# Optimization experiments

Measured on AMD Instinct MI355X. Metric: run time of the kernel, lower is better.

The kernel has to match this reference:

```python
import jax, jax.numpy as jnp
import numpy as np

N_NODES = 1024
HID = 128
NODE_D = 133
BOND_D = 14
E_HALF = 8192  # directed edges; doubled with reverses -> 16384


def setup_inputs() -> dict:
    key = jax.random.key(0)
    ks = jax.random.split(key, 24)

    x = jax.random.normal(ks[0], (N_NODES, NODE_D), jnp.float32)
    edge_attr = jax.random.normal(ks[1], (2 * E_HALF, BOND_D), jnp.float32)
    src = jax.random.randint(ks[2], (E_HALF,), 0, N_NODES)
    dst = jax.random.randint(ks[3], (E_HALF,), 0, N_NODES)
    # bidirectional edges so every edge has a reverse (as _rev_edge_index assumes)
    edge_index = jnp.stack([jnp.concatenate([src, dst]), jnp.concatenate([dst, src])]).astype(jnp.int32)
    rev_edge_index = jnp.concatenate([jnp.arange(E_HALF) + E_HALF, jnp.arange(E_HALF)]).astype(jnp.int32)

    dissociable_masks = (jax.random.uniform(ks[4], (N_NODES,)) < 0.1).astype(jnp.int32)
    pka_raw = jax.random.uniform(ks[5], (N_NODES,), minval=0.0, maxval=14.0)
    valid = jax.random.uniform(ks[6], (N_NODES,)) < (1.0 / 16.0)
    pka_values = jnp.where(valid, pka_raw, jnp.nan).astype(jnp.float32)

    def lin(k, fi, fo):
        return (jax.random.normal(k, (fi, fo)) / np.sqrt(fi)).astype(jnp.float32)

    z = lambda n: jnp.zeros((n,), jnp.float32)
    inp = dict(x=x, edge_attr=edge_attr, pka_values=pka_values,
               dissociable_masks=dissociable_masks, edge_index=edge_index,
               rev_edge_index=rev_edge_index,
               Wi=lin(ks[7], NODE_D + BOND_D, HID), bi=z(HID),
               Wh=lin(ks[8], HID, HID), bh=z(HID),
               Wo=lin(ks[9], NODE_D + HID, HID), bo=z(HID),
               Wnt=lin(ks[10], NODE_D, HID), bnt=z(HID),
               Wc1=lin(ks[11], HID, 256), bc1=z(256),
               Wc2=lin(ks[12], 256, 64), bc2=z(64),
               Wc3=lin(ks[13], 64, 2), bc3=z(2),
               Wr1=lin(ks[14], HID, 256), br1=z(256),
               Wr2=lin(ks[15], 256, 64), br2=z(64),
               Wr3=lin(ks[16], 64, 1), br3=z(1),
               Wg=lin(ks[17], HID, HID), bg=z(HID))
    return inp


def reference(x, edge_attr, pka_values, dissociable_masks, edge_index, rev_edge_index,
              Wi, bi, Wh, bh, Wo, bo, Wnt, bnt,
              Wc1, bc1, Wc2, bc2, Wc3, bc3,
              Wr1, br1, Wr2, br2, Wr3, br3, Wg, bg):
    n = x.shape[0]
    src, dst = edge_index[0], edge_index[1]

    # ---- BondMessagePassing (depth=3, dropout in eval mode) ----
    H0 = jnp.concatenate([x[src], edge_attr], axis=1) @ Wi + bi  # [E, HID]
    Ht = jax.nn.relu(H0)
    for _ in range(2):  # depth - 1 iterations
        agg = jax.ops.segment_sum(Ht, dst, num_segments=n)       # scatter-sum to dst
        M = agg[src] - Ht[rev_edge_index]                        # exclude reverse edge
        Ht = jax.nn.relu(H0 + M @ Wh + bh)
    agg = jax.ops.segment_sum(Ht, dst, num_segments=n)
    tx = x @ Wnt + bnt
    M = jnp.where(jnp.sum(agg, axis=1, keepdims=True) == 0, tx, agg)
    E = jax.nn.relu(jnp.concatenate([x, M], axis=1) @ Wo + bo)   # node embeddings [N, HID]

    valid = ~jnp.isnan(pka_values)
    pka_s = jnp.where(valid, pka_values, 0.0)

    def mlp(e, W1, b1, W2, b2, W3, b3):
        h = jax.nn.relu(e @ W1 + b1)
        h = jax.nn.relu(h @ W2 + b2)
        return h @ W3 + b3

    def step(carry, inp):
        Emb, cls_sum, reg_sum, correct = carry
        i, m_i, p_i, v_i = inp
        e = Emb[i]
        logits = mlp(e, Wc1, bc1, Wc2, bc2, Wc3, bc3)            # [2]
        label = jnp.argmax(logits).astype(jnp.int32)
        target = (m_i > 0).astype(jnp.int32)
        ce = -jax.nn.log_softmax(logits)[target]
        correct = correct + (label == target).astype(jnp.float32)
        reg_cond = (label == 1) | (m_i > 0)
        # sigmoid -> Hardtanh(0,14) (clip is identity on (0,1), kept for fidelity)
        p = jnp.clip(jax.nn.sigmoid(mlp(e, Wr1, br1, Wr2, br2, Wr3, br3))[0], 0.0, 14.0)
        fire = reg_cond & v_i
        reg_sum = reg_sum + jnp.where(fire, (p - p_i) ** 2, 0.0)
        Emb = jax.lax.cond(fire,
                           lambda A: A * (1.0 - jax.nn.sigmoid(A @ Wg + bg)),
                           lambda A: A, Emb)
        return (Emb, cls_sum + ce, reg_sum, correct), (label, jnp.where(reg_cond, p, 0.0))

    init = (E, jnp.float32(0.0), jnp.float32(0.0), jnp.float32(0.0))
    xs = (jnp.arange(n), dissociable_masks, pka_s, valid)
    (_, cls_sum, reg_sum, correct), (labels, preds) = jax.lax.scan(step, init, xs)
    acc = jax.lax.stop_gradient(correct / n)
    loss_vec = jnp.stack([cls_sum + reg_sum, cls_sum, reg_sum, acc])
    return labels, preds, loss_vec
```

## Files before the change

kernel.cpp:

```cpp
#include <hip/hip_runtime.h>

#define NN   1024
#define NE   16384
#define HID  128
#define ND   133
#define BD   14
#define KIN  147
#define NVMAX 128
#define EB   8
#define JF   4
#define JT   2
#define MAXPAIRS (NVMAX * (NVMAX + 1) / 2)
#define TB4 ((MAXPAIRS + JT - 1) / JT)

__device__ __forceinline__ float sigm(float x) { return 1.0f / (1.0f + expf(-x)); }


__global__ void __launch_bounds__(1024)
k_prep3(const int* __restrict__ dst, int* offs, int* elist,
        const float* __restrict__ pka, int* validIdx, int* NvP, int* vpos,
        const int* __restrict__ mask, int* pairCnt, int* pairList,
        int* lossTicket) {
    __shared__ int degS[NN];
    __shared__ int s2[NN];
    __shared__ int fillS[NN];
    __shared__ int elistS[NE];
    __shared__ int vIdxS[NVMAX];
    __shared__ int maskS[NVMAX];
    __shared__ int nvS, pcS;
    int t = threadIdx.x;
    degS[t] = 0;
    float v = pka[t];
    int f = (v == v) ? 1 : 0;
    s2[t] = f;
    __syncthreads();
    for (int e = t; e < NE; e += NN) atomicAdd(&degS[dst[e]], 1);
    __syncthreads();
    int d0 = degS[t];
    __syncthreads();
    for (int st = 1; st < NN; st <<= 1) {
        int a = (t >= st) ? degS[t - st] : 0;
        int b = (t >= st) ? s2[t - st] : 0;
        __syncthreads();
        degS[t] += a; s2[t] += b;
        __syncthreads();
    }
    int hi = degS[t];
    int lo = hi - d0;
    offs[t] = lo;
    fillS[t] = lo;
    if (t == NN - 1) offs[NN] = hi;
    int pos = s2[t] - f;
    int ok = (f && pos < NVMAX) ? 1 : 0;
    vpos[t] = ok ? pos : -1;
    if (ok) { validIdx[pos] = t; vIdxS[pos] = t; }
    if (t == NN - 1) { int nv = (s2[t] > NVMAX) ? NVMAX : s2[t]; *NvP = nv; nvS = nv; }
    if (t == 0) { pcS = 0; *lossTicket = 0; }
    __syncthreads();
    for (int e = t; e < NE; e += NN) { int p = atomicAdd(&fillS[dst[e]], 1); elistS[p] = e; }
    int Nv = nvS;
    if (t < NVMAX) maskS[t] = (t < Nv) ? mask[vIdxS[t]] : 1;
    __syncthreads();
    for (int a = lo + 1; a < hi; a++) {
        int vv = elistS[a]; int b = a - 1;
        while (b >= lo && elistS[b] > vv) { elistS[b + 1] = elistS[b]; b--; }
        elistS[b + 1] = vv;
    }
    for (int idx = t; idx < NVMAX * NVMAX; idx += NN) {
        int vv = idx >> 7, k = idx & (NVMAX - 1);
        if (vv < Nv && k <= vv && maskS[vv] == 0) {
            int p = atomicAdd(&pcS, 1);
            pairList[p] = idx;
        }
    }
    __syncthreads();
    if (t == 0) *pairCnt = pcS;
    for (int e = t; e < NE; e += NN) elist[e] = elistS[e];
}


__global__ void k_edge_init(const float* __restrict__ x, const float* __restrict__ ea,
                            const int* __restrict__ src,
                            const float* __restrict__ Wi, const float* __restrict__ bi,
                            float* __restrict__ H0, float* __restrict__ Ht) {
    __shared__ float in[EB][KIN + 1];
    int e0 = blockIdx.x * EB;
    int h = threadIdx.x;
    for (int j = 0; j < EB; j++) {
        int e = e0 + j; int s = src[e];
        for (int k = h; k < KIN; k += HID)
            in[j][k] = (k < ND) ? x[s * ND + k] : ea[e * BD + (k - ND)];
    }
    __syncthreads();
    float acc[EB];
#pragma unroll
    for (int j = 0; j < EB; j++) acc[j] = 0.f;
    for (int k4 = 0; k4 < KIN / 4; k4++) {
        float w0 = Wi[(4 * k4 + 0) * HID + h];
        float w1 = Wi[(4 * k4 + 1) * HID + h];
        float w2 = Wi[(4 * k4 + 2) * HID + h];
        float w3 = Wi[(4 * k4 + 3) * HID + h];
#pragma unroll
        for (int j = 0; j < EB; j++) {
            const float4 m4 = *(const float4*)&in[j][4 * k4];
            acc[j] = fmaf(m4.x, w0, acc[j]);
            acc[j] = fmaf(m4.y, w1, acc[j]);
            acc[j] = fmaf(m4.z, w2, acc[j]);
            acc[j] = fmaf(m4.w, w3, acc[j]);
        }
    }
    for (int k = (KIN / 4) * 4; k < KIN; k++) {
        float w = Wi[k * HID + h];
#pragma unroll
        for (int j = 0; j < EB; j++) acc[j] = fmaf(in[j][k], w, acc[j]);
    }
    float b = bi[h];
    for (int j = 0; j < EB; j++) {
        float v = acc[j] + b;
        H0[(e0 + j) * HID + h] = v;
        Ht[(e0 + j) * HID + h] = fmaxf(v, 0.f);
    }
}

__global__ void k_segsum(const float* __restrict__ Ht, const int* __restrict__ elist,
                         const int* __restrict__ offs, float* __restrict__ agg) {
    int n = blockIdx.x; int h = threadIdx.x;
    int lo = offs[n], hi = offs[n + 1];
    float a = 0.f;
    for (int j = lo; j < hi; j++) {
        int e = elist[j];
        a += Ht[e * HID + h];
    }
    agg[n * HID + h] = a;
}

__global__ void k_edge_update(const float* __restrict__ H0, const float* __restrict__ Htin,
                              const float* __restrict__ agg,
                              const int* __restrict__ src, const int* __restrict__ rev,
                              const float* __restrict__ Wh, const float* __restrict__ bh,
                              float* __restrict__ Htout) {
    __shared__ float M[EB][HID];
    int e0 = blockIdx.x * EB;
    int h = threadIdx.x;
    for (int j = 0; j < EB; j++) {
        int e = e0 + j; int s = src[e]; int r = rev[e];
        M[j][h] = agg[s * HID + h] - Htin[r * HID + h];
    }
    __syncthreads();
    float acc[EB];
#pragma unroll
    for (int j = 0; j < EB; j++) acc[j] = 0.f;
    for (int k4 = 0; k4 < HID / 4; k4++) {
        float w0 = Wh[(4 * k4 + 0) * HID + h];
        float w1 = Wh[(4 * k4 + 1) * HID + h];
        float w2 = Wh[(4 * k4 + 2) * HID + h];
        float w3 = Wh[(4 * k4 + 3) * HID + h];
#pragma unroll
        for (int j = 0; j < EB; j++) {
            const float4 m4 = *(const float4*)&M[j][4 * k4];
            acc[j] = fmaf(m4.x, w0, acc[j]);
            acc[j] = fmaf(m4.y, w1, acc[j]);
            acc[j] = fmaf(m4.z, w2, acc[j]);
            acc[j] = fmaf(m4.w, w3, acc[j]);
        }
    }
    float b = bh[h];
    for (int j = 0; j < EB; j++) {
        int e = e0 + j;
        Htout[e * HID + h] = fmaxf(H0[e * HID + h] + acc[j] + b, 0.f);
    }
}

__global__ void k_node_embed2(const float* __restrict__ x, const float* __restrict__ Ht,
                              const int* __restrict__ elist, const int* __restrict__ offs,
                              const float* __restrict__ Wnt, const float* __restrict__ bnt,
                              const float* __restrict__ Wo, const float* __restrict__ bo,
                              float* __restrict__ Emb) {
    __shared__ float xs[ND + 1];
    __shared__ float Ms[HID];
    __shared__ float red[HID];
    int n = blockIdx.x; int h = threadIdx.x;
    for (int k = h; k < ND; k += HID) xs[k] = x[n * ND + k];
    int lo = offs[n], hi = offs[n + 1];
    float a = 0.f;
    for (int j = lo; j < hi; j++) a += Ht[elist[j] * HID + h];
    red[h] = a;
    __syncthreads();
    for (int st = 64; st > 0; st >>= 1) { if (h < st) red[h] += red[h + st]; __syncthreads(); }
    float s = red[0];
    __syncthreads();
    float Mh;
    if (s == 0.0f) {
        float t0 = 0.f, t1 = 0.f;
        int k = 0;
        for (; k + 1 < ND; k += 2) {
            t0 = fmaf(xs[k], Wnt[k * HID + h], t0);
            t1 = fmaf(xs[k + 1], Wnt[(k + 1) * HID + h], t1);
        }
        for (; k < ND; k++) t0 = fmaf(xs[k], Wnt[k * HID + h], t0);
        Mh = (t0 + t1) + bnt[h];
    } else {
        Mh = a;
    }
    Ms[h] = Mh;
    __syncthreads();
    float a0 = 0.f, a1 = 0.f;
    int k = 0;
    for (; k + 1 < ND; k += 2) {
        a0 = fmaf(xs[k], Wo[k * HID + h], a0);
        a1 = fmaf(xs[k + 1], Wo[(k + 1) * HID + h], a1);
    }
    for (; k < ND; k++) a0 = fmaf(xs[k], Wo[k * HID + h], a0);
    for (int q = 0; q < HID; q += 2) {
        a0 = fmaf(Ms[q], Wo[(ND + q) * HID + h], a0);
        a1 = fmaf(Ms[q + 1], Wo[(ND + q + 1) * HID + h], a1);
    }
    Emb[n * HID + h] = fmaxf((a0 + a1) + bo[h], 0.f);
}


__global__ void __launch_bounds__(512)
k_chains3(const float* __restrict__ Emb, const int* __restrict__ validIdx,
          const int* __restrict__ NvP,
          const float* __restrict__ Wg, const float* __restrict__ bg,
          float* __restrict__ specSt) {
    int v = blockIdx.x;
    int Nv = *NvP;
    if (v >= Nv) return;
    __shared__ float rS[HID];
    __shared__ float pS[512];
    int tid = threadIdx.x;
    int col = tid & (HID - 1);
    int slot = tid >> 7;
    float wreg[32];
#pragma unroll
    for (int q = 0; q < 32; q++)
        wreg[q] = Wg[(slot * 32 + q) * HID + col];
    float bgc = bg[col];
    int i = validIdx[v];
    if (tid < HID) rS[tid] = Emb[i * HID + tid];
    __syncthreads();
    if (slot == 0) specSt[(size_t)(v * NVMAX + 0) * HID + col] = rS[col];
    int kmax = (v < NVMAX - 1) ? v : (NVMAX - 1);
    for (int k = 1; k <= kmax; k++) {
        const float4* r4 = (const float4*)&rS[slot * 32];
        float px = 0.f, py = 0.f, pz = 0.f, pw = 0.f;
#pragma unroll
        for (int q8 = 0; q8 < 8; q8++) {
            float4 rr = r4[q8];
            px = fmaf(rr.x, wreg[4 * q8 + 0], px);
            py = fmaf(rr.y, wreg[4 * q8 + 1], py);
            pz = fmaf(rr.z, wreg[4 * q8 + 2], pz);
            pw = fmaf(rr.w, wreg[4 * q8 + 3], pw);
        }
        pS[tid] = (px + py) + (pz + pw);
        __syncthreads();
        if (slot == 0) {
            float s = ((pS[col] + pS[col + 128]) + (pS[col + 256] + pS[col + 384])) + bgc;
            float g = 1.0f - sigm(s);
            float nr = rS[col] * g;
            rS[col] = nr;
            specSt[(size_t)(v * NVMAX + k) * HID + col] = nr;
        }
        __syncthreads();
    }
}


__global__ void __launch_bounds__(256)
k_table4(const float* __restrict__ specSt, const int* __restrict__ pairList,
         const int* __restrict__ pairCnt,
         const float* __restrict__ Wc1, const float* __restrict__ bc1,
         const float* __restrict__ Wc2, const float* __restrict__ bc2,
         const float* __restrict__ Wc3, const float* __restrict__ bc3,
         int* __restrict__ labTab) {
    int cnt = *pairCnt;
    int base = blockIdx.x * JT;
    if (base >= cnt) return;
    int nj = cnt - base; if (nj > JT) nj = JT;
    __shared__ float rS[JT][HID];
    __shared__ float h1S[JT][256];
    __shared__ float h2S[JT][64];
    __shared__ int plS[JT];
    int tid = threadIdx.x;
    if (tid < JT) plS[tid] = (tid < nj) ? pairList[base + tid] : 0;
    __syncthreads();
    for (int idx = tid; idx < JT * HID; idx += 256) {
        int j = idx >> 7, k = idx & (HID - 1);
        rS[j][k] = (j < nj) ? specSt[(size_t)plS[j] * HID + k] : 0.f;
    }
    __syncthreads();
    {
        float a[JT];
#pragma unroll
        for (int j = 0; j < JT; j++) a[j] = 0.f;
        for (int k = 0; k < HID; k++) {
            float w = Wc1[k * 256 + tid];
#pragma unroll
            for (int j = 0; j < JT; j++) a[j] = fmaf(rS[j][k], w, a[j]);
        }
        float b1 = bc1[tid];
#pragma unroll
        for (int j = 0; j < JT; j++) h1S[j][tid] = fmaxf(a[j] + b1, 0.f);
    }
    __syncthreads();
    {
        int col = tid & 63, j = tid >> 6;
        if (j < nj) {
            float acc = 0.f;
            for (int k = 0; k < 256; k++)
                acc = fmaf(h1S[j][k], Wc2[k * 64 + col], acc);
            h2S[j][col] = fmaxf(acc + bc2[col], 0.f);
        }
    }
    __syncthreads();
    if (tid < nj) {
        float l0 = bc3[0], l1 = bc3[1];
        for (int k = 0; k < 64; k++) {
            float h = h2S[tid][k];
            l0 = fmaf(h, Wc3[2 * k + 0], l0);
            l1 = fmaf(h, Wc3[2 * k + 1], l1);
        }
        labTab[plS[tid]] = (l1 > l0) ? 1 : 0;
    }
}


__global__ void k_resolve2(const int* __restrict__ validIdx, const int* __restrict__ NvP,
                           const int* __restrict__ mask, const int* __restrict__ labTab,
                           int* fireFlag, int* kPref) {
    __shared__ int vIdxS[NVMAX];
    __shared__ int maskS[NVMAX];
    __shared__ int labS[NVMAX * NVMAX];
    __shared__ int fireS[NN];
    __shared__ int scanS[NN];
    int t = threadIdx.x;
    int Nv = *NvP;
    if (t < NVMAX) {
        int vi = (t < Nv) ? validIdx[t] : 0;
        vIdxS[t] = vi;
        maskS[t] = (t < Nv) ? mask[vi] : 0;
    }
    fireS[t] = 0;
    for (int idx = t; idx < Nv * NVMAX; idx += NN) labS[idx] = labTab[idx];
    __syncthreads();
    if (t == 0) {
        int k = 0;
        for (int v = 0; v < Nv; v++) {
            int fire = (maskS[v] > 0) ? 1 : labS[v * NVMAX + k];
            fireS[vIdxS[v]] = fire;
            k += fire;
        }
    }
    __syncthreads();
    int f0 = fireS[t];
    scanS[t] = f0;
    __syncthreads();
    for (int st = 1; st < NN; st <<= 1) {
        int u = (t >= st) ? scanS[t - st] : 0;
        __syncthreads();
        scanS[t] += u;
        __syncthreads();
    }
    kPref[t] = scanS[t] - f0;
    fireFlag[t] = f0;
}


__global__ void __launch_bounds__(256)
k_final8(const float* __restrict__ Emb, const int* __restrict__ kPref,
         const int* __restrict__ fireFlag, const int* __restrict__ mask,
         const float* __restrict__ pka, const int* __restrict__ vpos,
         const int* __restrict__ labTab,
         const float* __restrict__ Wg, const float* __restrict__ bg,
         const float* __restrict__ Wc1, const float* __restrict__ bc1,
         const float* __restrict__ Wc2, const float* __restrict__ bc2,
         const float* __restrict__ Wc3, const float* __restrict__ bc3,
         const float* __restrict__ Wr1, const float* __restrict__ br1,
         const float* __restrict__ Wr2, const float* __restrict__ br2,
         const float* __restrict__ Wr3, const float* __restrict__ br3,
         float* __restrict__ outLabels, float* __restrict__ outPreds,
         float* __restrict__ ceArr, float* __restrict__ regArr,
         float* __restrict__ corArr, float* __restrict__ outLoss,
         int* __restrict__ lossTicket) {
    __shared__ __align__(16) float WgS[HID * HID];
    __shared__ __align__(16) float rS[JF][HID];
    __shared__ __align__(16) float pS[JF][8][HID];
    __shared__ float h1S[JF][256];
    __shared__ float h2S[JF][64];
    __shared__ float lgS[JF][2];
    __shared__ float prS[JF];
    __shared__ int kcS[JF];
    __shared__ int tkS;
    int tid = threadIdx.x;
    int i0 = blockIdx.x * JF;

    const float4* Wg4 = (const float4*)Wg;
    float4* Ws4 = (float4*)WgS;
    for (int idx = tid; idx < HID * HID / 4; idx += 256) Ws4[idx] = Wg4[idx];
    if (tid < HID) {
#pragma unroll
        for (int j = 0; j < JF; j++) rS[j][tid] = Emb[(i0 + j) * HID + tid];
    }
    if (tid < JF) kcS[tid] = kPref[i0 + tid];
    __syncthreads();
    int kc[JF]; int maxkc = 0;
#pragma unroll
    for (int j = 0; j < JF; j++) { kc[j] = kcS[j]; if (kc[j] > maxkc) maxkc = kc[j]; }

    int cg = tid & 31;
    int qs = tid >> 5;
    int q0 = qs * 16;
    int rc = tid & (HID - 1);
    int rh = tid >> 7;
    float bgc = bg[rc];
    const float4* WgS4 = (const float4*)WgS;
    for (int t = 0; t < maxkc; t++) {
        float4 acc[JF];
#pragma unroll
        for (int j = 0; j < JF; j++) acc[j] = make_float4(0.f, 0.f, 0.f, 0.f);
        for (int qq = 0; qq < 16; qq += 4) {
            int q = q0 + qq;
            const float4 w0 = WgS4[(q + 0) * 32 + cg];
            const float4 w1 = WgS4[(q + 1) * 32 + cg];
            const float4 w2 = WgS4[(q + 2) * 32 + cg];
            const float4 w3 = WgS4[(q + 3) * 32 + cg];
#pragma unroll
            for (int j = 0; j < JF; j++) {
                const float4 r = *(const float4*)&rS[j][q];
                acc[j].x = fmaf(r.x, w0.x, acc[j].x);
                acc[j].x = fmaf(r.y, w1.x, acc[j].x);
                acc[j].x = fmaf(r.z, w2.x, acc[j].x);
                acc[j].x = fmaf(r.w, w3.x, acc[j].x);
                acc[j].y = fmaf(r.x, w0.y, acc[j].y);
                acc[j].y = fmaf(r.y, w1.y, acc[j].y);
                acc[j].y = fmaf(r.z, w2.y, acc[j].y);
                acc[j].y = fmaf(r.w, w3.y, acc[j].y);
                acc[j].z = fmaf(r.x, w0.z, acc[j].z);
                acc[j].z = fmaf(r.y, w1.z, acc[j].z);
                acc[j].z = fmaf(r.z, w2.z, acc[j].z);
                acc[j].z = fmaf(r.w, w3.z, acc[j].z);
                acc[j].w = fmaf(r.x, w0.w, acc[j].w);
                acc[j].w = fmaf(r.y, w1.w, acc[j].w);
                acc[j].w = fmaf(r.z, w2.w, acc[j].w);
                acc[j].w = fmaf(r.w, w3.w, acc[j].w);
            }
        }
#pragma unroll
        for (int j = 0; j < JF; j++)
            *(float4*)&pS[j][qs][4 * cg] = acc[j];
        __syncthreads();
        float nr0, nr1;
        {
            int j = 2 * rh;
            float s = pS[j][0][rc];
#pragma unroll
            for (int z = 1; z < 8; z++) s += pS[j][z][rc];
            float g = 1.0f - sigm(s + bgc);
            nr0 = (t < kc[j]) ? rS[j][rc] * g : rS[j][rc];
        }
        {
            int j = 2 * rh + 1;
            float s = pS[j][0][rc];
#pragma unroll
            for (int z = 1; z < 8; z++) s += pS[j][z][rc];
            float g = 1.0f - sigm(s + bgc);
            nr1 = (t < kc[j]) ? rS[j][rc] * g : rS[j][rc];
        }
        __syncthreads();
        rS[2 * rh][rc] = nr0;
        rS[2 * rh + 1][rc] = nr1;
        __syncthreads();
    }

    {
        float a[JF];
#pragma unroll
        for (int j = 0; j < JF; j++) a[j] = 0.f;
        for (int k = 0; k < HID; k++) {
            float w = Wc1[k * 256 + tid];
#pragma unroll
            for (int j = 0; j < JF; j++) a[j] = fmaf(rS[j][k], w, a[j]);
        }
        float b = bc1[tid];
#pragma unroll
        for (int j = 0; j < JF; j++) h1S[j][tid] = fmaxf(a[j] + b, 0.f);
    }
    __syncthreads();
    {
        int c2 = tid & 63, j = tid >> 6;
        float acc = 0.f;
        for (int k = 0; k < 256; k++) acc = fmaf(h1S[j][k], Wc2[k * 64 + c2], acc);
        h2S[j][c2] = fmaxf(acc + bc2[c2], 0.f);
    }
    __syncthreads();
    if (tid < 2 * JF) {
        int j = tid >> 1, c = tid & 1;
        float l = bc3[c];
        for (int k = 0; k < 64; k++) l = fmaf(h2S[j][k], Wc3[2 * k + c], l);
        lgS[j][c] = l;
    }
    __syncthreads();

    {
        float a[JF];
#pragma unroll
        for (int j = 0; j < JF; j++) a[j] = 0.f;
        for (int k = 0; k < HID; k++) {
            float w = Wr1[k * 256 + tid];
#pragma unroll
            for (int j = 0; j < JF; j++) a[j] = fmaf(rS[j][k], w, a[j]);
        }
        float b = br1[tid];
#pragma unroll
        for (int j = 0; j < JF; j++) h1S[j][tid] = fmaxf(a[j] + b, 0.f);
    }
    __syncthreads();
    {
        int c2 = tid & 63, j = tid >> 6;
        float acc = 0.f;
        for (int k = 0; k < 256; k++) acc = fmaf(h1S[j][k], Wr2[k * 64 + c2], acc);
        h2S[j][c2] = fmaxf(acc + br2[c2], 0.f);
    }
    __syncthreads();
    if (tid < JF) {
        float pr = br3[0];
        for (int k = 0; k < 64; k++) pr = fmaf(h2S[tid][k], Wr3[k], pr);
        prS[tid] = pr;
    }
    __syncthreads();

    if (tid < JF) {
        int j = tid, i = i0 + j;
        float l0 = lgS[j][0], l1 = lgS[j][1];
        int compLab = (l1 > l0) ? 1 : 0;
        int vp = vpos[i];
        int label = (vp >= 0 && mask[i] == 0) ? labTab[vp * NVMAX + kc[j]] : compLab;
        int target = (mask[i] > 0) ? 1 : 0;
        float mx = fmaxf(l0, l1);
        float lse = mx + logf(expf(l0 - mx) + expf(l1 - mx));
        float ce = lse - ((target == 1) ? l1 : l0);
        int reg_cond = (label == 1) || (mask[i] > 0);
        float p = sigm(prS[j]);
        p = fminf(fmaxf(p, 0.f), 14.f);
        outLabels[i] = (float)label;
        outPreds[i] = reg_cond ? p : 0.f;
        ceArr[i] = ce;
        corArr[i] = (label == target) ? 1.f : 0.f;
        if (fireFlag[i]) {
            float d = p - pka[i];
            regArr[i] = d * d;
        } else {
            regArr[i] = 0.f;
        }
    }

    __threadfence();
    __syncthreads();
    if (tid == 0) tkS = atomicAdd(lossTicket, 1);
    __syncthreads();
    if (tkS == (NN / JF) - 1) {
        __threadfence();
        __shared__ float s[256];
        float a = ((ceArr[tid] + ceArr[tid + 256]) + (ceArr[tid + 512] + ceArr[tid + 768]));
        s[tid] = a; __syncthreads();
        for (int st = 128; st > 0; st >>= 1) { if (tid < st) s[tid] += s[tid + st]; __syncthreads(); }
        float cls = s[0]; __syncthreads();
        a = ((regArr[tid] + regArr[tid + 256]) + (regArr[tid + 512] + regArr[tid + 768]));
        s[tid] = a; __syncthreads();
        for (int st = 128; st > 0; st >>= 1) { if (tid < st) s[tid] += s[tid + st]; __syncthreads(); }
        float reg = s[0]; __syncthreads();
        a = ((corArr[tid] + corArr[tid + 256]) + (corArr[tid + 512] + corArr[tid + 768]));
        s[tid] = a; __syncthreads();
        for (int st = 128; st > 0; st >>= 1) { if (tid < st) s[tid] += s[tid + st]; __syncthreads(); }
        float cor = s[0];
        if (tid == 0) {
            outLoss[0] = cls + reg;
            outLoss[1] = cls;
            outLoss[2] = reg;
            outLoss[3] = cor / (float)NN;
        }
    }
}


extern "C" void kernel_launch(void* const* d_in, const int* in_sizes, int n_in,
                              void* d_out, int out_size, void* d_ws, size_t ws_size,
                              hipStream_t stream) {
    const float* x    = (const float*)d_in[0];
    const float* ea   = (const float*)d_in[1];
    const float* pka  = (const float*)d_in[2];
    const int*   mask = (const int*)d_in[3];
    const int*   eidx = (const int*)d_in[4];
    const int*   rev  = (const int*)d_in[5];
    const float* Wi  = (const float*)d_in[6];  const float* bi  = (const float*)d_in[7];
    const float* Wh  = (const float*)d_in[8];  const float* bh  = (const float*)d_in[9];
    const float* Wo  = (const float*)d_in[10]; const float* bo  = (const float*)d_in[11];
    const float* Wnt = (const float*)d_in[12]; const float* bnt = (const float*)d_in[13];
    const float* Wc1 = (const float*)d_in[14]; const float* bc1 = (const float*)d_in[15];
    const float* Wc2 = (const float*)d_in[16]; const float* bc2 = (const float*)d_in[17];
    const float* Wc3 = (const float*)d_in[18]; const float* bc3 = (const float*)d_in[19];
    const float* Wr1 = (const float*)d_in[20]; const float* br1 = (const float*)d_in[21];
    const float* Wr2 = (const float*)d_in[22]; const float* br2 = (const float*)d_in[23];
    const float* Wr3 = (const float*)d_in[24]; const float* br3 = (const float*)d_in[25];
    const float* Wg  = (const float*)d_in[26]; const float* bg  = (const float*)d_in[27];

    const int* src = eidx;
    const int* dst = eidx + NE;

    char* w = (char*)d_ws;
    auto alloc = [&](size_t bytes) -> void* {
        void* p = (void*)w;
        w += ((bytes + 255) / 256) * 256;
        return p;
    };
    float* H0   = (float*)alloc((size_t)NE * HID * 4);
    float* HtA  = (float*)alloc((size_t)NE * HID * 4);
    float* HtB  = (float*)alloc((size_t)NE * HID * 4);
    float* agg  = (float*)alloc((size_t)NN * HID * 4);
    float* Emb  = (float*)alloc((size_t)NN * HID * 4);
    int* offs    = (int*)alloc((NN + 1) * 4);
    int* elist   = (int*)alloc(NE * 4);
    int* validIdx= (int*)alloc(NVMAX * 4);
    int* NvP     = (int*)alloc(16);
    int* vpos    = (int*)alloc(NN * 4);
    int* fireFlag= (int*)alloc(NN * 4);
    int* kPref   = (int*)alloc(NN * 4);
    float* specSt= (float*)alloc((size_t)NVMAX * NVMAX * HID * 4);
    int* labTab  = (int*)alloc(NVMAX * NVMAX * 4);
    int* pairCnt = (int*)alloc(16);
    int* pairList= (int*)alloc(MAXPAIRS * 4);
    int* lossTicket = (int*)alloc(16);
    float* ceArr = (float*)alloc(NN * 4);
    float* regArr= (float*)alloc(NN * 4);
    float* corArr= (float*)alloc(NN * 4);

    float* outF = (float*)d_out;

    k_prep3<<<1, NN, 0, stream>>>(dst, offs, elist, pka, validIdx, NvP, vpos,
                                  mask, pairCnt, pairList, lossTicket);

    k_edge_init<<<NE / EB, HID, 0, stream>>>(x, ea, src, Wi, bi, H0, HtA);
    k_segsum<<<NN, HID, 0, stream>>>(HtA, elist, offs, agg);
    k_edge_update<<<NE / EB, HID, 0, stream>>>(H0, HtA, agg, src, rev, Wh, bh, HtB);
    k_segsum<<<NN, HID, 0, stream>>>(HtB, elist, offs, agg);
    k_edge_update<<<NE / EB, HID, 0, stream>>>(H0, HtB, agg, src, rev, Wh, bh, HtA);
    k_node_embed2<<<NN, HID, 0, stream>>>(x, HtA, elist, offs, Wnt, bnt, Wo, bo, Emb);

    k_chains3<<<NVMAX, 512, 0, stream>>>(Emb, validIdx, NvP, Wg, bg, specSt);
    k_table4<<<TB4, 256, 0, stream>>>(specSt, pairList, pairCnt,
                                      Wc1, bc1, Wc2, bc2, Wc3, bc3, labTab);
    k_resolve2<<<1, NN, 0, stream>>>(validIdx, NvP, mask, labTab, fireFlag, kPref);

    k_final8<<<NN / JF, 256, 0, stream>>>(Emb, kPref, fireFlag, mask, pka, vpos, labTab,
                                          Wg, bg, Wc1, bc1, Wc2, bc2, Wc3, bc3,
                                          Wr1, br1, Wr2, br2, Wr3, br3,
                                          outF, outF + NN, ceArr, regArr, corArr,
                                          outF + 2 * NN, lossTicket);
}
```

Baseline: 215.5 us.

## Double block size in final kernel and double-buffer gating state to drop a barrier

The final per-node kernel now runs 512 threads per block instead of 256. Each half of the block computes the gated matvec for two of the four nodes, and the first MLP layer is split the same way. The gating state is double-buffered, so each serial gating step needs two barriers instead of three. The aim is to shorten the serial chain of gating steps by spreading it over more threads. The cost is larger shared-memory use per block and some idle threads in the layers that stay 256-wide.

Result: slower. 225.5 us (+4.7%).

```diff
diff --git a/kernel.cpp b/kernel.cpp
--- a/kernel.cpp
+++ b/kernel.cpp
@@ -367,8 +367,8 @@
 }
 
 
-__global__ void __launch_bounds__(256)
-k_final8(const float* __restrict__ Emb, const int* __restrict__ kPref,
+__global__ void __launch_bounds__(512)
+k_final9(const float* __restrict__ Emb, const int* __restrict__ kPref,
          const int* __restrict__ fireFlag, const int* __restrict__ mask,
          const float* __restrict__ pka, const int* __restrict__ vpos,
          const int* __restrict__ labTab,
@@ -384,7 +384,7 @@
          float* __restrict__ corArr, float* __restrict__ outLoss,
          int* __restrict__ lossTicket) {
     __shared__ __align__(16) float WgS[HID * HID];
-    __shared__ __align__(16) float rS[JF][HID];
+    __shared__ __align__(16) float rs[2][JF][HID];
     __shared__ __align__(16) float pS[JF][8][HID];
     __shared__ float h1S[JF][256];
     __shared__ float h2S[JF][64];
@@ -397,10 +397,10 @@
 
     const float4* Wg4 = (const float4*)Wg;
     float4* Ws4 = (float4*)WgS;
-    for (int idx = tid; idx < HID * HID / 4; idx += 256) Ws4[idx] = Wg4[idx];
+    for (int idx = tid; idx < HID * HID / 4; idx += 512) Ws4[idx] = Wg4[idx];
     if (tid < HID) {
 #pragma unroll
-        for (int j = 0; j < JF; j++) rS[j][tid] = Emb[(i0 + j) * HID + tid];
+        for (int j = 0; j < JF; j++) rs[0][j][tid] = Emb[(i0 + j) * HID + tid];
     }
     if (tid < JF) kcS[tid] = kPref[i0 + tid];
     __syncthreads();
@@ -408,86 +408,80 @@
 #pragma unroll
     for (int j = 0; j < JF; j++) { kc[j] = kcS[j]; if (kc[j] > maxkc) maxkc = kc[j]; }
 
-    int cg = tid & 31;
-    int qs = tid >> 5;
+    int nh = tid >> 8;
+    int rem = tid & 255;
+    int cg = rem & 31;
+    int qs = rem >> 5;
     int q0 = qs * 16;
     int rc = tid & (HID - 1);
-    int rh = tid >> 7;
+    int rj = (tid >> 7) & 3;
     float bgc = bg[rc];
     const float4* WgS4 = (const float4*)WgS;
+    int cur = 0;
     for (int t = 0; t < maxkc; t++) {
-        float4 acc[JF];
-#pragma unroll
-        for (int j = 0; j < JF; j++) acc[j] = make_float4(0.f, 0.f, 0.f, 0.f);
+        int j0 = nh * 2, j1 = nh * 2 + 1;
+        float4 a0 = make_float4(0.f, 0.f, 0.f, 0.f);
+        float4 a1 = make_float4(0.f, 0.f, 0.f, 0.f);
         for (int qq = 0; qq < 16; qq += 4) {
             int q = q0 + qq;
             const float4 w0 = WgS4[(q + 0) * 32 + cg];
             const float4 w1 = WgS4[(q + 1) * 32 + cg];
             const float4 w2 = WgS4[(q + 2) * 32 + cg];
             const float4 w3 = WgS4[(q + 3) * 32 + cg];
-#pragma unroll
-            for (int j = 0; j < JF; j++) {
-                const float4 r = *(const float4*)&rS[j][q];
-                acc[j].x = fmaf(r.x, w0.x, acc[j].x);
-                acc[j].x = fmaf(r.y, w1.x, acc[j].x);
-                acc[j].x = fmaf(r.z, w2.x, acc[j].x);
-                acc[j].x = fmaf(r.w, w3.x, acc[j].x);
-                acc[j].y = fmaf(r.x, w0.y, acc[j].y);
-                acc[j].y = fmaf(r.y, w1.y, acc[j].y);
-                acc[j].y = fmaf(r.z, w2.y, acc[j].y);
-                acc[j].y = fmaf(r.w, w3.y, acc[j].y);
-                acc[j].z = fmaf(r.x, w0.z, acc[j].z);
-                acc[j].z = fmaf(r.y, w1.z, acc[j].z);
-                acc[j].z = fmaf(r.z, w2.z, acc[j].z);
-                acc[j].z = fmaf(r.w, w3.z, acc[j].z);
-                acc[j].w = fmaf(r.x, w0.w, acc[j].w);
-                acc[j].w = fmaf(r.y, w1.w, acc[j].w);
-                acc[j].w = fmaf(r.z, w2.w, acc[j].w);
-                acc[j].w = fmaf(r.w, w3.w, acc[j].w);
+            {
+                const float4 r = *(const float4*)&rs[cur][j0][q];
+                a0.x = fmaf(r.x, w0.x, a0.x); a0.x = fmaf(r.y, w1.x, a0.x);
+                a0.x = fmaf(r.z, w2.x, a0.x); a0.x = fmaf(r.w, w3.x, a0.x);
+                a0.y = fmaf(r.x, w0.y, a0.y); a0.y = fmaf(r.y, w1.y, a0.y);
+                a0.y = fmaf(r.z, w2.y, a0.y); a0.y = fmaf(r.w, w3.y, a0.y);
+                a0.z = fmaf(r.x, w0.z, a0.z); a0.z = fmaf(r.y, w1.z, a0.z);
+                a0.z = fmaf(r.z, w2.z, a0.z); a0.z = fmaf(r.w, w3.z, a0.z);
+                a0.w = fmaf(r.x, w0.w, a0.w); a0.w = fmaf(r.y, w1.w, a0.w);
+                a0.w = fmaf(r.z, w2.w, a0.w); a0.w = fmaf(r.w, w3.w, a0.w);
             }
-        }
-#pragma unroll
-        for (int j = 0; j < JF; j++)
-            *(float4*)&pS[j][qs][4 * cg] = acc[j];
-        __syncthreads();
-        float nr0, nr1;
+            {
+                const float4 r = *(const float4*)&rs[cur][j1][q];
+                a1.x = fmaf(r.x, w0.x, a1.x); a1.x = fmaf(r.y, w1.x, a1.x);
+                a1.x = fmaf(r.z, w2.x, a1.x); a1.x = fmaf(r.w, w3.x, a1.x);
+                a1.y = fmaf(r.x, w0.y, a1.y); a1.y = fmaf(r.y, w1.y, a1.y);
+                a1.y = fmaf(r.z, w2.y, a1.y); a1.y = fmaf(r.w, w3.y, a1.y);
+                a1.z = fmaf(r.x, w0.z, a1.z); a1.z = fmaf(r.y, w1.z, a1.z);
+                a1.z = fmaf(r.z, w2.z, a1.z); a1.z = fmaf(r.w, w3.z, a1.z);
+                a1.w = fmaf(r.x, w0.w, a1.w); a1.w = fmaf(r.y, w1.w, a1.w);
+                a1.w = fmaf(r.z, w2.w, a1.w); a1.w = fmaf(r.w, w3.w, a1.w);
+            }
+        }
+        *(float4*)&pS[j0][qs][4 * cg] = a0;
+        *(float4*)&pS[j1][qs][4 * cg] = a1;
+        __syncthreads();
         {
-            int j = 2 * rh;
-            float s = pS[j][0][rc];
-#pragma unroll
-            for (int z = 1; z < 8; z++) s += pS[j][z][rc];
+            float s = pS[rj][0][rc];
+#pragma unroll
+            for (int z = 1; z < 8; z++) s += pS[rj][z][rc];
             float g = 1.0f - sigm(s + bgc);
-            nr0 = (t < kc[j]) ? rS[j][rc] * g : rS[j][rc];
-        }
-        {
-            int j = 2 * rh + 1;
-            float s = pS[j][0][rc];
-#pragma unroll
-            for (int z = 1; z < 8; z++) s += pS[j][z][rc];
-            float g = 1.0f - sigm(s + bgc);
-            nr1 = (t < kc[j]) ? rS[j][rc] * g : rS[j][rc];
-        }
-        __syncthreads();
-        rS[2 * rh][rc] = nr0;
-        rS[2 * rh + 1][rc] = nr1;
-        __syncthreads();
-    }
+            float old = rs[cur][rj][rc];
+            rs[cur ^ 1][rj][rc] = (t < kc[rj]) ? old * g : old;
+        }
+        __syncthreads();
+        cur ^= 1;
+    }
+    const float (*rS)[HID] = rs[cur];
 
     {
-        float a[JF];
-#pragma unroll
-        for (int j = 0; j < JF; j++) a[j] = 0.f;
+        int half = tid >> 8, c = tid & 255;
+        int ja = half * 2, jb2 = half * 2 + 1;
+        float aa = 0.f, ab = 0.f;
         for (int k = 0; k < HID; k++) {
-            float w = Wc1[k * 256 + tid];
-#pragma unroll
-            for (int j = 0; j < JF; j++) a[j] = fmaf(rS[j][k], w, a[j]);
-        }
-        float b = bc1[tid];
-#pragma unroll
-        for (int j = 0; j < JF; j++) h1S[j][tid] = fmaxf(a[j] + b, 0.f);
-    }
-    __syncthreads();
-    {
+            float w = Wc1[k * 256 + c];
+            aa = fmaf(rS[ja][k], w, aa);
+            ab = fmaf(rS[jb2][k], w, ab);
+        }
+        float b = bc1[c];
+        h1S[ja][c] = fmaxf(aa + b, 0.f);
+        h1S[jb2][c] = fmaxf(ab + b, 0.f);
+    }
+    __syncthreads();
+    if (tid < 256) {
         int c2 = tid & 63, j = tid >> 6;
         float acc = 0.f;
         for (int k = 0; k < 256; k++) acc = fmaf(h1S[j][k], Wc2[k * 64 + c2], acc);
@@ -503,20 +497,20 @@
     __syncthreads();
 
     {
-        float a[JF];
-#pragma unroll
-        for (int j = 0; j < JF; j++) a[j] = 0.f;
+        int half = tid >> 8, c = tid & 255;
+        int ja = half * 2, jb2 = half * 2 + 1;
+        float aa = 0.f, ab = 0.f;
         for (int k = 0; k < HID; k++) {
-            float w = Wr1[k * 256 + tid];
-#pragma unroll
-            for (int j = 0; j < JF; j++) a[j] = fmaf(rS[j][k], w, a[j]);
-        }
-        float b = br1[tid];
-#pragma unroll
-        for (int j = 0; j < JF; j++) h1S[j][tid] = fmaxf(a[j] + b, 0.f);
-    }
-    __syncthreads();
-    {
+            float w = Wr1[k * 256 + c];
+            aa = fmaf(rS[ja][k], w, aa);
+            ab = fmaf(rS[jb2][k], w, ab);
+        }
+        float b = br1[c];
+        h1S[ja][c] = fmaxf(aa + b, 0.f);
+        h1S[jb2][c] = fmaxf(ab + b, 0.f);
+    }
+    __syncthreads();
+    if (tid < 256) {
         int c2 = tid & 63, j = tid >> 6;
         float acc = 0.f;
         for (int k = 0; k < 256; k++) acc = fmaf(h1S[j][k], Wr2[k * 64 + c2], acc);
@@ -562,16 +556,23 @@
     if (tkS == (NN / JF) - 1) {
         __threadfence();
         __shared__ float s[256];
-        float a = ((ceArr[tid] + ceArr[tid + 256]) + (ceArr[tid + 512] + ceArr[tid + 768]));
-        s[tid] = a; __syncthreads();
+        float a = 0.f;
+        if (tid < 256)
+            a = ((ceArr[tid] + ceArr[tid + 256]) + (ceArr[tid + 512] + ceArr[tid + 768]));
+        if (tid < 256) s[tid] = a;
+        __syncthreads();
         for (int st = 128; st > 0; st >>= 1) { if (tid < st) s[tid] += s[tid + st]; __syncthreads(); }
         float cls = s[0]; __syncthreads();
-        a = ((regArr[tid] + regArr[tid + 256]) + (regArr[tid + 512] + regArr[tid + 768]));
-        s[tid] = a; __syncthreads();
+        if (tid < 256)
+            a = ((regArr[tid] + regArr[tid + 256]) + (regArr[tid + 512] + regArr[tid + 768]));
+        if (tid < 256) s[tid] = a;
+        __syncthreads();
         for (int st = 128; st > 0; st >>= 1) { if (tid < st) s[tid] += s[tid + st]; __syncthreads(); }
         float reg = s[0]; __syncthreads();
-        a = ((corArr[tid] + corArr[tid + 256]) + (corArr[tid + 512] + corArr[tid + 768]));
-        s[tid] = a; __syncthreads();
+        if (tid < 256)
+            a = ((corArr[tid] + corArr[tid + 256]) + (corArr[tid + 512] + corArr[tid + 768]));
+        if (tid < 256) s[tid] = a;
+        __syncthreads();
         for (int st = 128; st > 0; st >>= 1) { if (tid < st) s[tid] += s[tid + st]; __syncthreads(); }
         float cor = s[0];
         if (tid == 0) {
@@ -652,7 +653,7 @@
                                       Wc1, bc1, Wc2, bc2, Wc3, bc3, labTab);
     k_resolve2<<<1, NN, 0, stream>>>(validIdx, NvP, mask, labTab, fireFlag, kPref);
 
-    k_final8<<<NN / JF, 256, 0, stream>>>(Emb, kPref, fireFlag, mask, pka, vpos, labTab,
+    k_final9<<<NN / JF, 512, 0, stream>>>(Emb, kPref, fireFlag, mask, pka, vpos, labTab,
                                           Wg, bg, Wc1, bc1, Wc2, bc2, Wc3, bc3,
                                           Wr1, br1, Wr2, br2, Wr3, br3,
                                           outF, outF + NN, ceArr, regArr, corArr,
```
